# Kernel tuning notes

Hardware: AMD Instinct MI355X
Metric: run time of the kernel (lower is better)

## Reference

```python
import jax, jax.numpy as jnp
import numpy as np

B, S, L, D = 256, 32, 20, 512  # users, social neighbors, history length, embedding_dim
IN = 2 * D  # use_fea_user + use_fea_item = 2 feature blocks of dim D


def setup_inputs() -> dict:
    key = jax.random.key(0)
    ks = jax.random.split(key, 9)
    f = jnp.float32
    xav = lambda k, o, i: jax.random.normal(k, (o, i), f) * (2.0 / (o + i)) ** 0.5
    return {
        "self_users": jax.random.normal(ks[0], (B, 1, L, D), f),
        "self_items": jax.random.normal(ks[1], (B, 1, L, D), f),
        "self_mask": (jax.random.uniform(ks[2], (B, 1, L)) < 0.9).astype(f),
        "social_users": jax.random.normal(ks[3], (B, S, L, D), f),
        "social_items": jax.random.normal(ks[4], (B, S, L, D), f),
        "social_mask": (jax.random.uniform(ks[5], (B, S, L)) < 0.9).astype(f),
        "ml_user_w": xav(ks[6], D, IN),
        "ml_user_b": jnp.zeros((D,), f),
        "ml_social_w1": xav(ks[7], D, D),
        "ml_social_b1": jnp.zeros((D,), f),
        "ml_social_w2": xav(ks[8], 1, D),
    }


def _aggregate_items(users, items, mask):
    # masked mean over history dim L -> [B, N, 2D]
    ui = jnp.concatenate((users, items), axis=-1) * mask[..., None]
    return ui.sum(axis=2) / (mask.sum(axis=2, keepdims=True) + 1e-4)


def _aggregate_rate(embd, w1, b1, w2):
    # embd: [B, D] -> global batch-attention pooled [1, D]
    t = jax.nn.relu(embd @ w1.T + b1)       # [B, D]
    att = jax.nn.softmax(w2 @ t.T, axis=1)  # [1, B]
    return att @ embd                        # [1, D]


def reference(self_users, self_items, self_mask, social_users, social_items,
              social_mask, ml_user_w, ml_user_b, ml_social_w1, ml_social_b1,
              ml_social_w2):
    self_agg = _aggregate_items(self_users, self_items, self_mask)        # [B,1,2D]
    self_embd = jax.nn.relu(self_agg @ ml_user_w.T + ml_user_b)           # [B,1,D]
    social_agg = _aggregate_items(social_users, social_items, social_mask)  # [B,S,2D]
    social_embd = jax.nn.relu(social_agg @ ml_user_w.T + ml_user_b)       # [B,S,D]
    # bmm attention of self over social neighbors
    att = jax.nn.softmax(jnp.einsum('bod,bsd->bos', self_embd, social_embd), axis=2)
    social_attn = jnp.einsum('bos,bsd->bod', att, social_embd)            # [B,1,D]
    se = _aggregate_rate(self_embd[:, 0], ml_social_w1, ml_social_b1, ml_social_w2)
    so = _aggregate_rate(social_attn[:, 0], ml_social_w1, ml_social_b1, ml_social_w2)
    return (se, so)  # each [1, D]
```

## Files before the change

### kernel.cpp

```cpp
#include <hip/hip_runtime.h>
#include <hip/hip_bf16.h>
#include <stdint.h>

#define B_   256
#define S_   32
#define L_   20
#define D_   512
#define IN_  1024
#define M_ROWS 8448
#define NT   512
#define FBM  48
#define ETS  516

typedef __attribute__((ext_vector_type(4))) float f32x4;
typedef __attribute__((ext_vector_type(8))) short s16x8;

static __device__ __forceinline__ float wave_reduce_sum(float v) {
#pragma unroll
  for (int off = 32; off > 0; off >>= 1) v += __shfl_xor(v, off);
  return v;
}

__global__ __launch_bounds__(256) void agg_cvt_kernel(
    const float* __restrict__ self_users, const float* __restrict__ self_items,
    const float* __restrict__ self_mask,
    const float* __restrict__ soc_users, const float* __restrict__ soc_items,
    const float* __restrict__ soc_mask,
    const float* __restrict__ w,
    __hip_bfloat16* __restrict__ agg, __hip_bfloat16* __restrict__ wb) {
  int r = blockIdx.x;
  int tid = threadIdx.x;
  if (r >= 2 * M_ROWS) {
    int base = (r - 2 * M_ROWS) * 4096 + tid * 16;
#pragma unroll
    for (int u = 0; u < 4; ++u) {
      f32x4 v = *(const f32x4*)(w + base + u * 4);
      __hip_bfloat16 h[4] = {__float2bfloat16(v[0]), __float2bfloat16(v[1]),
                             __float2bfloat16(v[2]), __float2bfloat16(v[3])};
      *(ushort4*)(wb + base + u * 4) = *(const ushort4*)h;
    }
    return;
  }
  __shared__ __align__(16) float rowbuf[L_ * D_];
  int arr = r & 1;
  int row = r >> 1;
  const float* src;
  const float* mptr;
  if (row < B_) {
    src = (arr ? self_items : self_users) + (size_t)row * (L_ * D_);
    mptr = self_mask + (size_t)row * L_;
  } else {
    int idx = row - B_;
    src = (arr ? soc_items : soc_users) + (size_t)idx * (L_ * D_);
    mptr = soc_mask + (size_t)idx * L_;
  }
#pragma unroll
  for (int k = 0; k < 10; ++k) {
    int off = (k * 256 + tid) * 4;
    __builtin_amdgcn_global_load_lds(
        (const __attribute__((address_space(1))) void*)(src + off),
        (__attribute__((address_space(3))) void*)(rowbuf + off), 16, 0, 0);
  }
  float mk[L_];
  float msum = 1e-4f;
#pragma unroll
  for (int l = 0; l < L_; ++l) { mk[l] = mptr[l]; msum += mk[l]; }
  float inv = 1.0f / msum;
  __syncthreads();

  float a0 = 0.f, a1 = 0.f;
#pragma unroll
  for (int l = 0; l < L_; ++l) {
    float2 v = *(const float2*)&rowbuf[l * D_ + tid * 2];
    a0 += mk[l] * v.x;
    a1 += mk[l] * v.y;
  }
  a0 *= inv;
  a1 *= inv;
  __hip_bfloat16 h[2] = {__float2bfloat16(a0), __float2bfloat16(a1)};
  *(ushort2*)(agg + (size_t)row * IN_ + arr * D_ + tid * 2) = *(const ushort2*)h;
}

__global__ __launch_bounds__(512) void fused_kernel(
    const __hip_bfloat16* __restrict__ agg, const __hip_bfloat16* __restrict__ wb,
    const float* __restrict__ bias,
    const float* __restrict__ W1, const float* __restrict__ b1,
    const float* __restrict__ w2,
    float* __restrict__ selfE, float* __restrict__ social_attn,
    float* __restrict__ scores) {
  int b = blockIdx.x;
  int tid = threadIdx.x, lane = tid & 63, wid = tid >> 6;

  __shared__ __align__(16) char smem[FBM * ETS * 4];
  ushort* Asub = (ushort*)smem;
  ushort* Wsub = Asub + 3072;
  float* Et = (float*)smem;
  __shared__ float arow[NT];
  __shared__ float sc_sh[S_], att_sh[S_], wpS[8], wpA[8];

  int a_row = tid >> 3;
  int a_g   = (tid & 7) ^ (a_row & 7);
  int growv = (a_row >= 1 && a_row <= 32) ? (B_ + b * S_ + a_row - 1) : b;
  const ushort* aggp = (const ushort*)agg + (size_t)growv * IN_ + a_g * 8;
  const ushort* wbp = (const ushort*)wb;

  f32x4 acc[3][4];
#pragma unroll
  for (int i = 0; i < 3; ++i)
#pragma unroll
    for (int j = 0; j < 4; ++j) acc[i][j] = {0.f, 0.f, 0.f, 0.f};

  for (int kt = 0; kt < IN_; kt += 64) {
    __syncthreads();
    if (tid < 384)
      __builtin_amdgcn_global_load_lds(
          (const __attribute__((address_space(1))) void*)(aggp + kt),
          (__attribute__((address_space(3))) void*)(Asub + tid * 8), 16, 0, 0);
#pragma unroll
    for (int it = 0; it < 8; ++it) {
      int s = it * 512 + tid;
      int wrow = s >> 3;
      int wg = (s & 7) ^ (wrow & 7);
      __builtin_amdgcn_global_load_lds(
          (const __attribute__((address_space(1))) void*)(wbp + (size_t)wrow * IN_ + kt + wg * 8),
          (__attribute__((address_space(3))) void*)(Wsub + s * 8), 16, 0, 0);
    }
    __syncthreads();
#pragma unroll
    for (int kk = 0; kk < 64; kk += 32) {
      s16x8 af[3], bf[4];
#pragma unroll
      for (int i = 0; i < 3; ++i) {
        int row = i * 16 + (lane & 15);
        int g = ((kk >> 3) + (lane >> 4)) ^ (row & 7);
        af[i] = *(const s16x8*)(Asub + row * 64 + g * 8);
      }
#pragma unroll
      for (int j = 0; j < 4; ++j) {
        int wrow = wid * 64 + j * 16 + (lane & 15);
        int g = ((kk >> 3) + (lane >> 4)) ^ (wrow & 7);
        bf[j] = *(const s16x8*)(Wsub + wrow * 64 + g * 8);
      }
#pragma unroll
      for (int i = 0; i < 3; ++i)
#pragma unroll
        for (int j = 0; j < 4; ++j)
          acc[i][j] = __builtin_amdgcn_mfma_f32_16x16x32_bf16(af[i], bf[j], acc[i][j], 0, 0, 0);
    }
  }
  __syncthreads();

#pragma unroll
  for (int j = 0; j < 4; ++j) {
    int col = wid * 64 + j * 16 + (lane & 15);
    float bv = bias[col];
#pragma unroll
    for (int i = 0; i < 3; ++i) {
#pragma unroll
      for (int q = 0; q < 4; ++q) {
        int row = i * 16 + (lane >> 4) * 4 + q;
        float v = acc[i][j][q] + bv;
        Et[row * ETS + col] = v > 0.f ? v : 0.f;
      }
    }
  }
  __syncthreads();

  {
    f32x4 s0 = *(const f32x4*)&Et[lane * 8];
    f32x4 s1 = *(const f32x4*)&Et[lane * 8 + 4];
#pragma unroll
    for (int q = 0; q < 4; ++q) {
      int s = wid * 4 + q + 1;
      f32x4 v0 = *(const f32x4*)&Et[s * ETS + lane * 8];
      f32x4 v1 = *(const f32x4*)&Et[s * ETS + lane * 8 + 4];
      float p = s0[0]*v0[0] + s0[1]*v0[1] + s0[2]*v0[2] + s0[3]*v0[3]
              + s1[0]*v1[0] + s1[1]*v1[1] + s1[2]*v1[2] + s1[3]*v1[3];
      p = wave_reduce_sum(p);
      if (lane == 0) sc_sh[s - 1] = p;
    }
  }
  __syncthreads();
  if (wid == 0) {
    float v = (lane < S_) ? sc_sh[lane] : -3.4e38f;
    float m = v;
#pragma unroll
    for (int off = 16; off > 0; off >>= 1) m = fmaxf(m, __shfl_xor(m, off));
    float e = (lane < S_) ? expf(v - m) : 0.f;
    float sum = e;
#pragma unroll
    for (int off = 16; off > 0; off >>= 1) sum += __shfl_xor(sum, off);
    if (lane < S_) att_sh[lane] = e / sum;
  }
  __syncthreads();
  {
    float a = 0.f;
#pragma unroll 8
    for (int s = 1; s <= S_; ++s) a += att_sh[s - 1] * Et[s * ETS + tid];
    arow[tid] = a;
    social_attn[(size_t)b * NT + tid] = a;
    selfE[(size_t)b * NT + tid] = Et[tid];
  }
  __syncthreads();

  {
    f32x4 es0 = *(const f32x4*)&Et[lane * 8];
    f32x4 es1 = *(const f32x4*)&Et[lane * 8 + 4];
    f32x4 ea0 = *(const f32x4*)&arow[lane * 8];
    f32x4 ea1 = *(const f32x4*)&arow[lane * 8 + 4];
    float accS = 0.f, accA = 0.f;
    for (int r = wid; r < D_; r += 8) {
      const float* wr_ = W1 + (size_t)r * D_ + lane * 8;
      f32x4 w0 = *(const f32x4*)wr_;
      f32x4 w1v = *(const f32x4*)(wr_ + 4);
      float pS = es0[0]*w0[0] + es0[1]*w0[1] + es0[2]*w0[2] + es0[3]*w0[3]
               + es1[0]*w1v[0] + es1[1]*w1v[1] + es1[2]*w1v[2] + es1[3]*w1v[3];
      float pA = ea0[0]*w0[0] + ea0[1]*w0[1] + ea0[2]*w0[2] + ea0[3]*w0[3]
               + ea1[0]*w1v[0] + ea1[1]*w1v[1] + ea1[2]*w1v[2] + ea1[3]*w1v[3];
#pragma unroll
      for (int off = 32; off > 0; off >>= 1) {
        pS += __shfl_xor(pS, off);
        pA += __shfl_xor(pA, off);
      }
      float bv = b1[r], wv = w2[r];
      float tS = pS + bv; tS = tS > 0.f ? tS : 0.f;
      float tA = pA + bv; tA = tA > 0.f ? tA : 0.f;
      accS += wv * tS;
      accA += wv * tA;
    }
    if (lane == 0) { wpS[wid] = accS; wpA[wid] = accA; }
  }
  __syncthreads();
  if (tid == 0) {
    float s = 0.f;
#pragma unroll
    for (int k = 0; k < 8; ++k) s += wpS[k];
    scores[b] = s;
  }
  if (tid == 1) {
    float s = 0.f;
#pragma unroll
    for (int k = 0; k < 8; ++k) s += wpA[k];
    scores[B_ + b] = s;
  }
}

__global__ __launch_bounds__(256) void pool_partial_kernel(
    const float* __restrict__ selfE, const float* __restrict__ social_attn,
    const float* __restrict__ scores, float* __restrict__ partial) {
  int v = blockIdx.x >> 3;
  int chunk = blockIdx.x & 7;
  const float* E = v ? social_attn : selfE;
  const float* sc = scores + v * B_;
  __shared__ float att[B_];
  __shared__ float red[8];
  int tid = threadIdx.x, lane = tid & 63, wid = tid >> 6;
  float s = sc[tid];
  float m = s;
#pragma unroll
  for (int off = 32; off > 0; off >>= 1) m = fmaxf(m, __shfl_xor(m, off));
  if (lane == 0) red[wid] = m;
  __syncthreads();
  m = fmaxf(fmaxf(red[0], red[1]), fmaxf(red[2], red[3]));
  float ev = expf(s - m);
  float sum = wave_reduce_sum(ev);
  if (lane == 0) red[4 + wid] = sum;
  __syncthreads();
  sum = red[4] + red[5] + red[6] + red[7];
  att[tid] = ev / sum;
  __syncthreads();
  float a0 = 0.f, a1 = 0.f;
#pragma unroll 8
  for (int q = 0; q < 32; ++q) {
    int b = chunk * 32 + q;
    float w = att[b];
    a0 += w * E[(size_t)b * NT + tid];
    a1 += w * E[(size_t)b * NT + tid + 256];
  }
  partial[(size_t)blockIdx.x * NT + tid] = a0;
  partial[(size_t)blockIdx.x * NT + tid + 256] = a1;
}

__global__ __launch_bounds__(256) void pool_final_kernel(
    const float* __restrict__ partial, float* __restrict__ out) {
  int v = blockIdx.x;
  int tid = threadIdx.x;
  float a0 = 0.f, a1 = 0.f;
#pragma unroll
  for (int c = 0; c < 8; ++c) {
    const float* p = partial + (size_t)(v * 8 + c) * NT;
    a0 += p[tid];
    a1 += p[tid + 256];
  }
  out[v * NT + tid] = a0;
  out[v * NT + tid + 256] = a1;
}

extern "C" void kernel_launch(void* const* d_in, const int* in_sizes, int n_in,
                              void* d_out, int out_size, void* d_ws, size_t ws_size,
                              hipStream_t stream) {
  const float* self_users = (const float*)d_in[0];
  const float* self_items = (const float*)d_in[1];
  const float* self_mask  = (const float*)d_in[2];
  const float* soc_users  = (const float*)d_in[3];
  const float* soc_items  = (const float*)d_in[4];
  const float* soc_mask   = (const float*)d_in[5];
  const float* ml_user_w  = (const float*)d_in[6];
  const float* ml_user_b  = (const float*)d_in[7];
  const float* ml_w1      = (const float*)d_in[8];
  const float* ml_b1      = (const float*)d_in[9];
  const float* ml_w2      = (const float*)d_in[10];

  char* ws = (char*)d_ws;
  __hip_bfloat16* agg = (__hip_bfloat16*)ws;
  __hip_bfloat16* wb  = (__hip_bfloat16*)(ws + 17301504);
  float* selfE        = (float*)(ws + 18350080);
  float* social_attn  = (float*)(ws + 18874368);
  float* scores       = (float*)(ws + 19398656);
  float* partial      = (float*)(ws + 19400704);

  hipLaunchKernelGGL(agg_cvt_kernel, dim3(2 * M_ROWS + 128), dim3(256), 0, stream,
                     self_users, self_items, self_mask, soc_users, soc_items,
                     soc_mask, ml_user_w, agg, wb);
  hipLaunchKernelGGL(fused_kernel, dim3(B_), dim3(512), 0, stream,
                     agg, wb, ml_user_b, ml_w1, ml_b1, ml_w2,
                     selfE, social_attn, scores);
  hipLaunchKernelGGL(pool_partial_kernel, dim3(16), dim3(256), 0, stream,
                     selfE, social_attn, scores, partial);
  hipLaunchKernelGGL(pool_final_kernel, dim3(2), dim3(256), 0, stream,
                     partial, (float*)d_out);
}
```

Before: 198.3 us.

## Make aggregation kernel persistent with triple-buffered async LDS loads

Replaces the one-block-per-row aggregation with a persistent grid of 256 blocks. Each block loops over 66 row tasks and prefetches the next two tasks' history rows and masks into a triple-buffered LDS ring using async global-to-LDS loads, synchronised with explicit vmcnt waits. The goal is to keep memory streaming continuously instead of paying block launch and load latency for every row. The weight bf16 conversion moves to its own small kernel, which adds one launch. The large LDS footprint (about 123 KB) limits residency to one block per CU, so the hand-tuned vmcnt counts must stay correct for overlap and correctness to hold.

```diff
diff --git a/kernel.cpp b/kernel.cpp
--- a/kernel.cpp
+++ b/kernel.cpp
@@ -11,6 +11,7 @@
 #define NT   512
 #define FBM  48
 #define ETS  516
+#define GRID_AGG 256
 
 typedef __attribute__((ext_vector_type(4))) float f32x4;
 typedef __attribute__((ext_vector_type(8))) short s16x8;
@@ -21,64 +22,96 @@
   return v;
 }
 
-__global__ __launch_bounds__(256) void agg_cvt_kernel(
+__global__ __launch_bounds__(256) void agg_kernel(
     const float* __restrict__ self_users, const float* __restrict__ self_items,
     const float* __restrict__ self_mask,
     const float* __restrict__ soc_users, const float* __restrict__ soc_items,
     const float* __restrict__ soc_mask,
-    const float* __restrict__ w,
-    __hip_bfloat16* __restrict__ agg, __hip_bfloat16* __restrict__ wb) {
-  int r = blockIdx.x;
-  int tid = threadIdx.x;
-  if (r >= 2 * M_ROWS) {
-    int base = (r - 2 * M_ROWS) * 4096 + tid * 16;
-#pragma unroll
-    for (int u = 0; u < 4; ++u) {
-      f32x4 v = *(const f32x4*)(w + base + u * 4);
-      __hip_bfloat16 h[4] = {__float2bfloat16(v[0]), __float2bfloat16(v[1]),
-                             __float2bfloat16(v[2]), __float2bfloat16(v[3])};
-      *(ushort4*)(wb + base + u * 4) = *(const ushort4*)h;
-    }
-    return;
-  }
-  __shared__ __align__(16) float rowbuf[L_ * D_];
-  int arr = r & 1;
-  int row = r >> 1;
-  const float* src;
-  const float* mptr;
-  if (row < B_) {
-    src = (arr ? self_items : self_users) + (size_t)row * (L_ * D_);
-    mptr = self_mask + (size_t)row * L_;
-  } else {
-    int idx = row - B_;
-    src = (arr ? soc_items : soc_users) + (size_t)idx * (L_ * D_);
-    mptr = soc_mask + (size_t)idx * L_;
-  }
-#pragma unroll
-  for (int k = 0; k < 10; ++k) {
-    int off = (k * 256 + tid) * 4;
+    __hip_bfloat16* __restrict__ agg) {
+  __shared__ __align__(16) float buf[3][L_ * D_];
+  __shared__ __align__(16) float maskbuf[3][64];
+  const int tid = threadIdx.x;
+  const int lane = tid & 63;
+  const int nt = (2 * M_ROWS) / GRID_AGG;
+
+  auto stage = [&](int it, int nb) {
+    int task = blockIdx.x + it * GRID_AGG;
+    int row = task >> 1, arr = task & 1;
+    const float* src;
+    const float* mptr;
+    if (row < B_) {
+      src = (arr ? self_items : self_users) + (size_t)row * (L_ * D_);
+      mptr = self_mask + (size_t)row * L_;
+    } else {
+      int idx = row - B_;
+      src = (arr ? soc_items : soc_users) + (size_t)idx * (L_ * D_);
+      mptr = soc_mask + (size_t)idx * L_;
+    }
+    const float* msrc = mptr + (lane < L_ ? lane : L_ - 1);
     __builtin_amdgcn_global_load_lds(
-        (const __attribute__((address_space(1))) void*)(src + off),
-        (__attribute__((address_space(3))) void*)(rowbuf + off), 16, 0, 0);
-  }
-  float mk[L_];
-  float msum = 1e-4f;
-#pragma unroll
-  for (int l = 0; l < L_; ++l) { mk[l] = mptr[l]; msum += mk[l]; }
-  float inv = 1.0f / msum;
-  __syncthreads();
-
-  float a0 = 0.f, a1 = 0.f;
-#pragma unroll
-  for (int l = 0; l < L_; ++l) {
-    float2 v = *(const float2*)&rowbuf[l * D_ + tid * 2];
-    a0 += mk[l] * v.x;
-    a1 += mk[l] * v.y;
-  }
-  a0 *= inv;
-  a1 *= inv;
-  __hip_bfloat16 h[2] = {__float2bfloat16(a0), __float2bfloat16(a1)};
-  *(ushort2*)(agg + (size_t)row * IN_ + arr * D_ + tid * 2) = *(const ushort2*)h;
+        (const __attribute__((address_space(1))) void*)msrc,
+        (__attribute__((address_space(3))) void*)&maskbuf[nb][0], 4, 0, 0);
+#pragma unroll
+    for (int k = 0; k < 10; ++k) {
+      int off = (k * 256 + tid) * 4;
+      __builtin_amdgcn_global_load_lds(
+          (const __attribute__((address_space(1))) void*)(src + off),
+          (__attribute__((address_space(3))) void*)(&buf[nb][0] + off), 16, 0, 0);
+    }
+  };
+
+  stage(0, 0);
+  stage(1, 1);
+
+  for (int it = 0; it < nt; ++it) {
+    int cb = it % 3;
+    int task = blockIdx.x + it * GRID_AGG;
+    if (it + 2 < nt) {
+      stage(it + 2, (it + 2) % 3);
+      __builtin_amdgcn_sched_barrier(0);
+      asm volatile("s_waitcnt vmcnt(22)" ::: "memory");
+    } else if (it + 1 < nt) {
+      __builtin_amdgcn_sched_barrier(0);
+      asm volatile("s_waitcnt vmcnt(11)" ::: "memory");
+    } else {
+      __builtin_amdgcn_sched_barrier(0);
+      asm volatile("s_waitcnt vmcnt(0)" ::: "memory");
+    }
+    __builtin_amdgcn_sched_barrier(0);
+    __builtin_amdgcn_s_barrier();
+    __builtin_amdgcn_sched_barrier(0);
+
+    float mk[L_];
+    float msum = 1e-4f;
+#pragma unroll
+    for (int l = 0; l < L_; ++l) { mk[l] = maskbuf[cb][l]; msum += mk[l]; }
+    float inv = 1.0f / msum;
+    float a0 = 0.f, a1 = 0.f;
+#pragma unroll
+    for (int l = 0; l < L_; ++l) {
+      float2 v = *(const float2*)&buf[cb][l * D_ + tid * 2];
+      a0 += mk[l] * v.x;
+      a1 += mk[l] * v.y;
+    }
+    a0 *= inv;
+    a1 *= inv;
+    int row = task >> 1, arr = task & 1;
+    __hip_bfloat16 h[2] = {__float2bfloat16(a0), __float2bfloat16(a1)};
+    *(ushort2*)(agg + (size_t)row * IN_ + arr * D_ + tid * 2) = *(const ushort2*)h;
+
+    __builtin_amdgcn_sched_barrier(0);
+    __builtin_amdgcn_s_barrier();
+    __builtin_amdgcn_sched_barrier(0);
+  }
+}
+
+__global__ __launch_bounds__(256) void cvt_w_kernel(
+    const float* __restrict__ w, __hip_bfloat16* __restrict__ wb) {
+  int i = (blockIdx.x * 256 + threadIdx.x) * 4;
+  f32x4 v = *(const f32x4*)(w + i);
+  __hip_bfloat16 h[4] = {__float2bfloat16(v[0]), __float2bfloat16(v[1]),
+                         __float2bfloat16(v[2]), __float2bfloat16(v[3])};
+  *(ushort4*)(wb + i) = *(const ushort4*)h;
 }
 
 __global__ __launch_bounds__(512) void fused_kernel(
@@ -319,9 +352,10 @@
   float* scores       = (float*)(ws + 19398656);
   float* partial      = (float*)(ws + 19400704);
 
-  hipLaunchKernelGGL(agg_cvt_kernel, dim3(2 * M_ROWS + 128), dim3(256), 0, stream,
+  hipLaunchKernelGGL(agg_kernel, dim3(GRID_AGG), dim3(256), 0, stream,
                      self_users, self_items, self_mask, soc_users, soc_items,
-                     soc_mask, ml_user_w, agg, wb);
+                     soc_mask, agg);
+  hipLaunchKernelGGL(cvt_w_kernel, dim3(512), dim3(256), 0, stream, ml_user_w, wb);
   hipLaunchKernelGGL(fused_kernel, dim3(B_), dim3(512), 0, stream,
                      agg, wb, ml_user_b, ml_w1, ml_b1, ml_w2,
                      selfE, social_attn, scores);
```

Measured after the change: 249.9 us. 26.0% more time.
